# Optimization experiments

Hardware: AMD Instinct MI355X
Metric: run time of the kernel (lower is better)

Reference implementation:

```python
import jax, jax.numpy as jnp
import numpy as np

S, B, D, H = 1024, 8, 768, 12
PROMPT_NUM = 8
DH = D // H


def setup_inputs() -> dict:
    key = jax.random.key(0)
    ks = jax.random.split(key, 5)
    scale = 1.0 / np.sqrt(D)
    return {
        "x": jax.random.normal(ks[0], (S, B, D), dtype=jnp.float32),
        "in_proj_weight": jax.random.normal(ks[1], (3 * D, D), dtype=jnp.float32) * scale,
        "in_proj_bias": jax.random.normal(ks[2], (3 * D,), dtype=jnp.float32) * 0.02,
        "out_w": jax.random.normal(ks[3], (D, D), dtype=jnp.float32) * scale,
        "out_b": jax.random.normal(ks[4], (D,), dtype=jnp.float32) * 0.02,
    }


def reference(x, in_proj_weight, in_proj_bias, out_w, out_b):
    # x: (S, B, D) -> (B, S, D)
    xt = jnp.transpose(x, (1, 0, 2))
    qkv = xt @ in_proj_weight.T + in_proj_bias  # (B, S, 3D)
    q, k, v = jnp.split(qkv, 3, axis=-1)
    q = q.reshape(B, S, H, DH)
    k = k.reshape(B, S, H, DH)
    v = v.reshape(B, S, H, DH)
    # affinity (n, q, k, h); scale by sqrt(head_dim)
    aff = jnp.einsum("nqhc,nkhc->nqkh", q / np.sqrt(DH), k)
    # prompt masking: CLS_MASK | PROMPT_MASK
    tokens = S - PROMPT_NUM
    m = np.zeros((S, S), dtype=bool)
    m[0, tokens:] = True          # CLS_MASK: CLS query can't attend to prompts
    m[tokens:, tokens:] = True    # PROMPT_MASK: prompts can't attend to prompts
    m = jnp.asarray(m)
    aff = jnp.where(m[None, :, :, None], jnp.float32(-10000.0), aff)
    # softmax over key axis (dim=-2 of nqkh)
    aff = jax.nn.softmax(aff, axis=2)
    mix = jnp.einsum("nqlh,nlhc->nqhc", aff, v)  # (B, S, H, DH)
    out = mix.reshape(B, S, D) @ out_w.T + out_b
    # transpose back to (S, B, ...)
    return (
        jnp.transpose(q, (1, 0, 2, 3)),
        jnp.transpose(k, (1, 0, 2, 3)),
        jnp.transpose(v, (1, 0, 2, 3)),
        jnp.transpose(out, (1, 0, 2)),
    )
```

## Files before the change

kernel.cpp:

```cpp
#include <hip/hip_runtime.h>
#include <hip/hip_bf16.h>


typedef unsigned short u16;
typedef __attribute__((ext_vector_type(8))) short short8;
typedef __attribute__((ext_vector_type(4))) short short4v;
typedef __attribute__((ext_vector_type(4))) float floatx4;
typedef __attribute__((ext_vector_type(4))) unsigned short ushort4v;
typedef __attribute__((ext_vector_type(2))) unsigned int uint2v;

#define NB 8
#define NS 1024
#define NH 12
#define ND 768
#define DHD 64
#define TOKENS 1016
#define QKV_OUT_STRIDE 6291456

#if __has_builtin(__builtin_amdgcn_exp2f)
#define EXP2(x) __builtin_amdgcn_exp2f(x)
#else
#define EXP2(x) exp2f(x)
#endif

#if defined(__HIP_DEVICE_COMPILE__)
  #if __has_builtin(__builtin_amdgcn_mfma_f32_16x16x16bf16_1k)
    #define MFMA16(a, b, c) __builtin_amdgcn_mfma_f32_16x16x16bf16_1k(a, b, c, 0, 0, 0)
  #else
    #define MFMA16(a, b, c) __builtin_amdgcn_mfma_f32_16x16x16_bf16(a, b, c, 0, 0, 0)
  #endif
  #define GLD16(g, l)                                                        \
    __builtin_amdgcn_global_load_lds(                                        \
        (const __attribute__((address_space(1))) void*)(g),                  \
        (__attribute__((address_space(3))) void*)(l), 16, 0, 0)
  #define SETPRIO(n) __builtin_amdgcn_s_setprio(n)
#else
  #define MFMA16(a, b, c) (c)
  #define GLD16(g, l) ((void)0)
  #define SETPRIO(n) ((void)0)
#endif

__device__ __forceinline__ u16 f2bf(float f) {
  union { float f; unsigned u; } c; c.f = f;
  return (u16)((c.u + 0x7fffu + ((c.u >> 16) & 1u)) >> 16);
}

#define CVT_B0 6144
#define CVT_B1 1728
#define CVT_B2 576
__global__ __launch_bounds__(256) void cvt3(
    const float* __restrict__ s0, u16* __restrict__ d0,
    const float* __restrict__ s1, u16* __restrict__ d1,
    const float* __restrict__ s2, u16* __restrict__ d2) {
  int blk = blockIdx.x;
  if (blk < CVT_B0) {
    const int i = (blk * 256 + (int)threadIdx.x) * 4;
    const float4 v = *(const float4*)(s0 + i);
    const int sb = i / ND;
    const int dd = i - sb * ND;
    const int m = ((sb & 7) << 10) | (sb >> 3);
    ushort4v o;
    o.x = f2bf(v.x); o.y = f2bf(v.y); o.z = f2bf(v.z); o.w = f2bf(v.w);
    *(ushort4v*)(d0 + m * ND + dd) = o;
    return;
  }
  const float* s; u16* d;
  if (blk < CVT_B0 + CVT_B1) { s = s1; d = d1; blk -= CVT_B0; }
  else { s = s2; d = d2; blk -= CVT_B0 + CVT_B1; }
  const int i = (blk * 256 + (int)threadIdx.x) * 4;
  const float4 v = *(const float4*)(s + i);
  ushort4v o;
  o.x = f2bf(v.x); o.y = f2bf(v.y); o.z = f2bf(v.z); o.w = f2bf(v.w);
  *(ushort4v*)(d + i) = o;
}

#define GEMM_STAGE(buf, k0)                                                  \
  do {                                                                       \
    GLD16(ga0 + (k0), &buf##A[c0 * 16][0]);                                  \
    GLD16(ga1 + (k0), &buf##A[c0 * 16 + 16][0]);                             \
    GLD16(gb0 + (k0), &buf##B[c0 * 16][0]);                                  \
    GLD16(gb1 + (k0), &buf##B[c0 * 16 + 16][0]);                             \
  } while (0)

#define GEMM_COMPUTE(buf)                                                    \
  do {                                                                       \
    short8 af[4], bfr[4];                                                    \
    _Pragma("unroll")                                                        \
    for (int mt = 0; mt < 4; ++mt)                                           \
      af[mt] = *(const short8*)&buf##A[wm * 64 + mt * 16 + l15][quad * 8];   \
    _Pragma("unroll")                                                        \
    for (int nt = 0; nt < 4; ++nt)                                           \
      bfr[nt] = *(const short8*)&buf##B[wn * 64 + nt * 16 + l15][quad * 8];  \
    _Pragma("unroll")                                                        \
    for (int mt = 0; mt < 4; ++mt)                                           \
      _Pragma("unroll")                                                      \
      for (int nt = 0; nt < 4; ++nt)                                         \
        acc[mt][nt] = __builtin_amdgcn_mfma_f32_16x16x32_bf16(               \
            af[mt], bfr[nt], acc[mt][nt], 0, 0, 0);                          \
  } while (0)

__global__ __launch_bounds__(256) void qkv_gemm(
    const u16* __restrict__ Xb, const u16* __restrict__ Wb,
    const float* __restrict__ bias, float* __restrict__ out,
    u16* __restrict__ Kb) {
  __shared__ __align__(16) u16 p0A[128][32];
  __shared__ __align__(16) u16 p0B[128][32];
  __shared__ __align__(16) u16 p1A[128][32];
  __shared__ __align__(16) u16 p1B[128][32];
  const int tid = threadIdx.x;
  const int lane = tid & 63, wave = tid >> 6;
  const int l15 = lane & 15, quad = lane >> 4;
  const int wm = wave & 1, wn = wave >> 1;
  const int L = (int)blockIdx.x + 64 * (int)blockIdx.y;
  const int xcd = L & 7, i = L >> 3;
  const int mblk = (xcd + 8 * (i & 7)) * 128;
  const int nblk = (i >> 3) * 128;

  floatx4 acc[4][4];
#pragma unroll
  for (int i2 = 0; i2 < 4; ++i2)
#pragma unroll
    for (int j = 0; j < 4; ++j) acc[i2][j] = (floatx4)0.f;

  const int lr = lane >> 2;
  const int lc = (lane & 3) * 8;
  const int c0 = wave * 2;
  const int r0 = c0 * 16 + lr, r1 = r0 + 16;
  const u16* ga0 = Xb + (mblk + r0) * ND + lc;
  const u16* ga1 = Xb + (mblk + r1) * ND + lc;
  const u16* gb0 = Wb + (nblk + r0) * ND + lc;
  const u16* gb1 = Wb + (nblk + r1) * ND + lc;

  GEMM_STAGE(p0, 0);
  __syncthreads();
  for (int kt = 0; kt < 24; kt += 2) {
    GEMM_STAGE(p1, (kt + 1) * 32);
    GEMM_COMPUTE(p0);
    __syncthreads();
    if (kt + 2 < 24) GEMM_STAGE(p0, (kt + 2) * 32);
    GEMM_COMPUTE(p1);
    __syncthreads();
  }

  const int seg = nblk / ND;
  const int nbase = nblk - seg * ND;
  float* outp = out + seg * QKV_OUT_STRIDE;
#pragma unroll
  for (int mt = 0; mt < 4; ++mt) {
#pragma unroll
    for (int r = 0; r < 4; ++r) {
      const int gm = mblk + wm * 64 + mt * 16 + quad * 4 + r;
      const int b = gm >> 10, s = gm & 1023;
#pragma unroll
      for (int nt = 0; nt < 4; ++nt) {
        const int gn = nblk + wn * 64 + nt * 16 + l15;
        const int nn = nbase + wn * 64 + nt * 16 + l15;
        const float val = acc[mt][nt][r] + bias[gn];
        outp[(s * NB + b) * ND + nn] = val;
        if (seg == 1) {
          Kb[(((size_t)b * NH + (nn >> 6)) * NS + s) * DHD + (nn & 63)] =
              f2bf(val);
        }
      }
    }
  }
}

__global__ __launch_bounds__(256) void prep(
    const float* __restrict__ V, u16* __restrict__ Vt) {
  __shared__ u16 tile[DHD][40];
  const int t = threadIdx.x;
  const int bh = blockIdx.y;
  const int b = bh / NH, h = bh % NH;
  const int s0 = blockIdx.x * 32;
  const int sl = t >> 3;
  const int c0 = (t & 7) * 8;
  const int s = s0 + sl;
  const float* src = V + ((s * NB + b) * NH + h) * DHD + c0;
  const float4 v0 = *(const float4*)src;
  const float4 v1 = *(const float4*)(src + 4);
  tile[c0 + 0][sl] = f2bf(v0.x); tile[c0 + 1][sl] = f2bf(v0.y);
  tile[c0 + 2][sl] = f2bf(v0.z); tile[c0 + 3][sl] = f2bf(v0.w);
  tile[c0 + 4][sl] = f2bf(v1.x); tile[c0 + 5][sl] = f2bf(v1.y);
  tile[c0 + 6][sl] = f2bf(v1.z); tile[c0 + 7][sl] = f2bf(v1.w);
  __syncthreads();
  const int c = t >> 2;
  const int so = (t & 3) * 8;
  *(short8*)(Vt + ((size_t)bh * DHD + c) * NS + s0 + so) =
      *(const short8*)&tile[c][so];
}

__global__ __launch_bounds__(256) void attn(
    const float* __restrict__ Q, const u16* __restrict__ Kb,
    const u16* __restrict__ Vt, u16* __restrict__ mix) {
  __shared__ __align__(16) u16 Kt[128][72];
  __shared__ __align__(16) u16 Vs[64][136];
  const int tid = threadIdx.x;
  const int lane = tid & 63, wave = tid >> 6;
  const int l15 = lane & 15, quad = lane >> 4;
  const int L = (int)blockIdx.x + 8 * (int)blockIdx.y;
  const int xcd = L & 7, tt = L >> 3;
  const int bh = xcd + 8 * (tt >> 3);
  const int qx = tt & 7;
  const int b = bh / NH, h = bh % NH;
  const int qb = qx * 128 + wave * 32;

  const float SC = 0.125f * 1.44269504089f;

  short8 qf[2][2];
  bool qmask[2];
#pragma unroll
  for (int j = 0; j < 2; ++j) {
    const int qj = qb + j * 16 + l15;
    qmask[j] = (qj == 0 || qj >= TOKENS);
    const float* qp = Q + ((qj * NB + b) * NH + h) * DHD + quad * 8;
#pragma unroll
    for (int e = 0; e < 8; ++e) {
      qf[j][0][e] = (short)f2bf(qp[e] * SC);
      qf[j][1][e] = (short)f2bf(qp[32 + e] * SC);
    }
  }

  floatx4 O[2][4];
#pragma unroll
  for (int j = 0; j < 2; ++j)
#pragma unroll
    for (int g = 0; g < 4; ++g) O[j][g] = (floatx4)0.f;
  floatx4 liacc[2];
  liacc[0] = (floatx4)0.f;
  liacc[1] = (floatx4)0.f;
  short4v ones4;
#pragma unroll
  for (int e = 0; e < 4; ++e) ones4[e] = (short)0x3F80;

  const u16* kg = Kb + (size_t)bh * NS * DHD;
  const u16* vg = Vt + (size_t)bh * DHD * NS;

  const int krow = tid >> 1;
  const int kcol = (tid & 1) * 32;
  const int vrow = tid >> 2;
  const int vcol = (tid & 3) * 32;

  short8 pk[4], pv[4];
#pragma unroll
  for (int u = 0; u < 4; ++u) {
    pk[u] = *(const short8*)(kg + krow * DHD + kcol + u * 8);
    pv[u] = *(const short8*)(vg + vrow * NS + vcol + u * 8);
  }

  for (int it = 0; it < 8; ++it) {
#pragma unroll
    for (int u = 0; u < 4; ++u) {
      *(short8*)&Kt[krow][kcol + u * 8] = pk[u];
      *(short8*)&Vs[vrow][vcol + u * 8] = pv[u];
    }
    __syncthreads();
    if (it < 7) {
      const int k0 = (it + 1) * 128;
#pragma unroll
      for (int u = 0; u < 4; ++u) {
        pk[u] = *(const short8*)(kg + (k0 + krow) * DHD + kcol + u * 8);
        pv[u] = *(const short8*)(vg + vrow * NS + k0 + vcol + u * 8);
      }
    }
#pragma unroll
    for (int half = 0; half < 2; ++half) {
      const bool mrow = (it == 7) && (half == 1) && (quad >= 2);
#pragma unroll
      for (int sub = 0; sub < 4; ++sub) {
        const int kr = half * 64 + sub * 16 + l15;
        const short8 kf0 = *(const short8*)&Kt[kr][quad * 8];
        const short8 kf1 = *(const short8*)&Kt[kr][32 + quad * 8];
        short4v pb[2];
#pragma unroll
        for (int j = 0; j < 2; ++j) {
          floatx4 a = (floatx4)0.f;
          a = __builtin_amdgcn_mfma_f32_16x16x32_bf16(kf0, qf[j][0], a, 0, 0, 0);
          a = __builtin_amdgcn_mfma_f32_16x16x32_bf16(kf1, qf[j][1], a, 0, 0, 0);
          float p[4];
#pragma unroll
          for (int r = 0; r < 4; ++r) p[r] = EXP2(a[r]);
          if (sub == 3 && mrow && qmask[j]) {
#pragma unroll
            for (int r = 0; r < 4; ++r) p[r] = 0.f;
          }
          __hip_bfloat162 w0 = __float22bfloat162_rn(make_float2(p[0], p[1]));
          __hip_bfloat162 w1 = __float22bfloat162_rn(make_float2(p[2], p[3]));
          uint2v pw;
          pw.x = *(const unsigned*)&w0;
          pw.y = *(const unsigned*)&w1;
          pb[j] = __builtin_bit_cast(short4v, pw);
        }
        SETPRIO(1);
#pragma unroll
        for (int g = 0; g < 4; ++g) {
          const short4v vf =
              *(const short4v*)&Vs[g * 16 + l15][half * 64 + sub * 16 + quad * 4];
          O[0][g] = MFMA16(vf, pb[0], O[0][g]);
          O[1][g] = MFMA16(vf, pb[1], O[1][g]);
        }
        liacc[0] = MFMA16(ones4, pb[0], liacc[0]);
        liacc[1] = MFMA16(ones4, pb[1], liacc[1]);
        SETPRIO(0);
      }
    }
    __syncthreads();
  }

#pragma unroll
  for (int j = 0; j < 2; ++j) {
    const float rl = 1.0f / liacc[j][0];
    const int qj = qb + j * 16 + l15;
    u16* mp = mix + ((size_t)b * NS + qj) * ND + h * DHD + quad * 4;
#pragma unroll
    for (int g = 0; g < 4; ++g) {
      ushort4v o;
#pragma unroll
      for (int r = 0; r < 4; ++r) o[r] = f2bf(O[j][g][r] * rl);
      *(ushort4v*)(mp + g * 16) = o;
    }
  }
}

__global__ __launch_bounds__(256) void out_gemm(
    const u16* __restrict__ A, const u16* __restrict__ Wb,
    const float* __restrict__ bias, float* __restrict__ out) {
  __shared__ __align__(16) u16 p0A[128][32];
  __shared__ __align__(16) u16 p0B[128][32];
  __shared__ __align__(16) u16 p1A[128][32];
  __shared__ __align__(16) u16 p1B[128][32];
  const int tid = threadIdx.x;
  const int lane = tid & 63, wave = tid >> 6;
  const int l15 = lane & 15, quad = lane >> 4;
  const int wm = wave & 1, wn = wave >> 1;
  const int L = (int)blockIdx.x + 64 * (int)blockIdx.y;
  const int xcd = L & 7, i = L >> 3;
  const int mblk = (xcd + 8 * (i & 7)) * 128;
  const int nblk = (i >> 3) * 128;

  floatx4 acc[4][4];
#pragma unroll
  for (int i2 = 0; i2 < 4; ++i2)
#pragma unroll
    for (int j = 0; j < 4; ++j) acc[i2][j] = (floatx4)0.f;

  const int lr = lane >> 2;
  const int lc = (lane & 3) * 8;
  const int c0 = wave * 2;
  const int r0 = c0 * 16 + lr, r1 = r0 + 16;
  const u16* ga0 = A + (mblk + r0) * ND + lc;
  const u16* ga1 = A + (mblk + r1) * ND + lc;
  const u16* gb0 = Wb + (nblk + r0) * ND + lc;
  const u16* gb1 = Wb + (nblk + r1) * ND + lc;

  GEMM_STAGE(p0, 0);
  __syncthreads();
  for (int kt = 0; kt < 24; kt += 2) {
    GEMM_STAGE(p1, (kt + 1) * 32);
    GEMM_COMPUTE(p0);
    __syncthreads();
    if (kt + 2 < 24) GEMM_STAGE(p0, (kt + 2) * 32);
    GEMM_COMPUTE(p1);
    __syncthreads();
  }

#pragma unroll
  for (int mt = 0; mt < 4; ++mt) {
#pragma unroll
    for (int r = 0; r < 4; ++r) {
      const int gm = mblk + wm * 64 + mt * 16 + quad * 4 + r;
      const int b = gm >> 10, s = gm & 1023;
#pragma unroll
      for (int nt = 0; nt < 4; ++nt) {
        const int gn = nblk + wn * 64 + nt * 16 + l15;
        out[(s * NB + b) * ND + gn] = acc[mt][nt][r] + bias[gn];
      }
    }
  }
}

extern "C" void kernel_launch(void* const* d_in, const int* in_sizes, int n_in,
                              void* d_out, int out_size, void* d_ws, size_t ws_size,
                              hipStream_t stream) {
  const float* X  = (const float*)d_in[0];
  const float* W  = (const float*)d_in[1];
  const float* Bi = (const float*)d_in[2];
  const float* Ow = (const float*)d_in[3];
  const float* Ob = (const float*)d_in[4];
  float* out = (float*)d_out;

  u16* Xb  = (u16*)d_ws;
  u16* Wb  = Xb  + 6291456;
  u16* Owb = Wb  + 1769472;
  u16* Vt  = Owb + 589824;
  u16* Kb  = Vt  + 6291456;
  u16* mix = Kb  + 6291456;

  cvt3<<<CVT_B0 + CVT_B1 + CVT_B2, 256, 0, stream>>>(X, Xb, W, Wb, Ow, Owb);
  qkv_gemm<<<dim3(64, 18), 256, 0, stream>>>(Xb, Wb, Bi, out, Kb);
  prep<<<dim3(32, 96), 256, 0, stream>>>(out + 2 * QKV_OUT_STRIDE, Vt);
  attn<<<dim3(8, 96), 256, 0, stream>>>(out, Kb, Vt, mix);
  out_gemm<<<dim3(64, 6), 256, 0, stream>>>(mix, Owb, Ob, out + 3 * QKV_OUT_STRIDE);
}
```

Baseline: 232.1 us.

## Load K and V fragments directly from global memory in attention, dropping LDS staging

The attention kernel no longer stages K and V tiles through shared memory with register prefetch and block barriers. Each wave now loads its MFMA fragments straight from global memory (relying on L1/L2 cache) in a 64-step loop over 16-key slices. This removes LDS writes, LDS reads and the __syncthreads per tile. In exchange, the four waves of a block each fetch the same K/V data from cache, and the loop has no explicit prefetch, so global-load latency may be exposed before each MFMA.

```diff
diff --git a/kernel.cpp b/kernel.cpp
--- a/kernel.cpp
+++ b/kernel.cpp
@@ -193,8 +193,6 @@
 __global__ __launch_bounds__(256) void attn(
     const float* __restrict__ Q, const u16* __restrict__ Kb,
     const u16* __restrict__ Vt, u16* __restrict__ mix) {
-  __shared__ __align__(16) u16 Kt[128][72];
-  __shared__ __align__(16) u16 Vs[64][136];
   const int tid = threadIdx.x;
   const int lane = tid & 63, wave = tid >> 6;
   const int l15 = lane & 15, quad = lane >> 4;
@@ -236,75 +234,46 @@
   const u16* kg = Kb + (size_t)bh * NS * DHD;
   const u16* vg = Vt + (size_t)bh * DHD * NS;
 
-  const int krow = tid >> 1;
-  const int kcol = (tid & 1) * 32;
-  const int vrow = tid >> 2;
-  const int vcol = (tid & 3) * 32;
-
-  short8 pk[4], pv[4];
-#pragma unroll
-  for (int u = 0; u < 4; ++u) {
-    pk[u] = *(const short8*)(kg + krow * DHD + kcol + u * 8);
-    pv[u] = *(const short8*)(vg + vrow * NS + vcol + u * 8);
-  }
-
-  for (int it = 0; it < 8; ++it) {
-#pragma unroll
-    for (int u = 0; u < 4; ++u) {
-      *(short8*)&Kt[krow][kcol + u * 8] = pk[u];
-      *(short8*)&Vs[vrow][vcol + u * 8] = pv[u];
-    }
-    __syncthreads();
-    if (it < 7) {
-      const int k0 = (it + 1) * 128;
-#pragma unroll
-      for (int u = 0; u < 4; ++u) {
-        pk[u] = *(const short8*)(kg + (k0 + krow) * DHD + kcol + u * 8);
-        pv[u] = *(const short8*)(vg + vrow * NS + k0 + vcol + u * 8);
+  const u16* kp = kg + l15 * DHD + quad * 8;
+  const u16* vp = vg + l15 * NS + quad * 4;
+
+  for (int ks = 0; ks < 64; ++ks) {
+    const short8 kf0 = *(const short8*)(kp + ks * 16 * DHD);
+    const short8 kf1 = *(const short8*)(kp + ks * 16 * DHD + 32);
+    const bool mrow = (ks == 63) && (quad >= 2);
+    short4v pb[2];
+#pragma unroll
+    for (int j = 0; j < 2; ++j) {
+      floatx4 a = (floatx4)0.f;
+      a = __builtin_amdgcn_mfma_f32_16x16x32_bf16(kf0, qf[j][0], a, 0, 0, 0);
+      a = __builtin_amdgcn_mfma_f32_16x16x32_bf16(kf1, qf[j][1], a, 0, 0, 0);
+      float p[4];
+#pragma unroll
+      for (int r = 0; r < 4; ++r) p[r] = EXP2(a[r]);
+      if (mrow && qmask[j]) {
+#pragma unroll
+        for (int r = 0; r < 4; ++r) p[r] = 0.f;
       }
-    }
-#pragma unroll
-    for (int half = 0; half < 2; ++half) {
-      const bool mrow = (it == 7) && (half == 1) && (quad >= 2);
-#pragma unroll
-      for (int sub = 0; sub < 4; ++sub) {
-        const int kr = half * 64 + sub * 16 + l15;
-        const short8 kf0 = *(const short8*)&Kt[kr][quad * 8];
-        const short8 kf1 = *(const short8*)&Kt[kr][32 + quad * 8];
-        short4v pb[2];
-#pragma unroll
-        for (int j = 0; j < 2; ++j) {
-          floatx4 a = (floatx4)0.f;
-          a = __builtin_amdgcn_mfma_f32_16x16x32_bf16(kf0, qf[j][0], a, 0, 0, 0);
-          a = __builtin_amdgcn_mfma_f32_16x16x32_bf16(kf1, qf[j][1], a, 0, 0, 0);
-          float p[4];
-#pragma unroll
-          for (int r = 0; r < 4; ++r) p[r] = EXP2(a[r]);
-          if (sub == 3 && mrow && qmask[j]) {
-#pragma unroll
-            for (int r = 0; r < 4; ++r) p[r] = 0.f;
-          }
-          __hip_bfloat162 w0 = __float22bfloat162_rn(make_float2(p[0], p[1]));
-          __hip_bfloat162 w1 = __float22bfloat162_rn(make_float2(p[2], p[3]));
-          uint2v pw;
-          pw.x = *(const unsigned*)&w0;
-          pw.y = *(const unsigned*)&w1;
-          pb[j] = __builtin_bit_cast(short4v, pw);
-        }
-        SETPRIO(1);
-#pragma unroll
-        for (int g = 0; g < 4; ++g) {
-          const short4v vf =
-              *(const short4v*)&Vs[g * 16 + l15][half * 64 + sub * 16 + quad * 4];
-          O[0][g] = MFMA16(vf, pb[0], O[0][g]);
-          O[1][g] = MFMA16(vf, pb[1], O[1][g]);
-        }
-        liacc[0] = MFMA16(ones4, pb[0], liacc[0]);
-        liacc[1] = MFMA16(ones4, pb[1], liacc[1]);
-        SETPRIO(0);
-      }
-    }
-    __syncthreads();
+      __hip_bfloat162 w0 = __float22bfloat162_rn(make_float2(p[0], p[1]));
+      __hip_bfloat162 w1 = __float22bfloat162_rn(make_float2(p[2], p[3]));
+      uint2v pw;
+      pw.x = *(const unsigned*)&w0;
+      pw.y = *(const unsigned*)&w1;
+      pb[j] = __builtin_bit_cast(short4v, pw);
+    }
+    short4v vf[4];
+#pragma unroll
+    for (int g = 0; g < 4; ++g)
+      vf[g] = *(const short4v*)(vp + g * 16 * NS + ks * 16);
+    SETPRIO(1);
+#pragma unroll
+    for (int g = 0; g < 4; ++g) {
+      O[0][g] = MFMA16(vf[g], pb[0], O[0][g]);
+      O[1][g] = MFMA16(vf[g], pb[1], O[1][g]);
+    }
+    liacc[0] = MFMA16(ones4, pb[0], liacc[0]);
+    liacc[1] = MFMA16(ones4, pb[1], liacc[1]);
+    SETPRIO(0);
   }
 
 #pragma unroll
```

New measurement: 323.8 us. 39.5% more time.
